# Kernel tuning notes

Measured on AMD Instinct MI355X. Metric: run time of the kernel, lower is better.

Reference implementation:

```python
import jax, jax.numpy as jnp
import numpy as np

H, C = 4, 32            # heads, hidden_channel
HC = H * C              # 128
IN = 128                # in_channel
N = 50000               # nodes in sampled subgraph
E = 200000              # edges
USER, ITEM = 50000, 50000
UB = 200                # ubias_num == ibias_num
DIST = 501
BATCH = 1024
NEG = 0.2               # leaky_relu negative slope


def setup_inputs() -> dict:
    key = jax.random.key(0)
    keys = iter(jax.random.split(key, 64))

    def nrm(shape):
        return jax.random.normal(next(keys), shape, dtype=jnp.float32) * 0.05

    def ri(shape, hi):
        return jax.random.randint(next(keys), shape, 0, hi, dtype=jnp.int32)

    inp = {
        # int (graph) inputs
        "node_idx": ri((N,), USER + ITEM + 1),
        "edge_index": ri((2, E), N),
        "edge_type": ri((E,), 6),
        "t_offset_0": ri((E,), UB + 2),
        "t_offset_1": ri((E,), UB + 2),
        "dists_0": ri((E,), DIST),
        "dists_1": ri((E,), DIST),
        "center_nid": ri((BATCH,), N),
        # parameters
        "id_emb": nrm((USER + ITEM + 1, IN)),
        "ucenter_att_bias": nrm((UB + 2, HC)),
        "icenter_att_bias": nrm((UB + 2, HC)),
        "trans_att_bias": nrm((UB + 2, HC)),
        "ucenter_emb_bias": nrm((UB + 2, HC)),
        "icenter_emb_bias": nrm((UB + 2, HC)),
        "trans_emb_bias": nrm((UB + 2, HC)),
        "ucenter_att_bias_2": nrm((UB * 4 + 2, HC)),
        "icenter_att_bias_2": nrm((UB * 4 + 2, HC)),
        "trans_att_bias_2": nrm((UB * 4 + 2, HC)),
        "ucenter_emb_bias_2": nrm((UB * 4 + 2, HC)),
        "icenter_emb_bias_2": nrm((UB * 4 + 2, HC)),
        "trans_emb_bias_2": nrm((UB * 4 + 2, HC)),
        "udist_att_bias": nrm((DIST, HC)),
        "idist_att_bias": nrm((DIST, HC)),
        "udist_emb_bias": nrm((DIST, HC)),
        "idist_emb_bias": nrm((DIST, HC)),
        "udist_att_bias_2": nrm((DIST, HC)),
        "idist_att_bias_2": nrm((DIST, HC)),
        "udist_emb_bias_2": nrm((DIST, HC)),
        "idist_emb_bias_2": nrm((DIST, HC)),
        "trans_head": nrm((IN, HC)),
        "rnn_w": nrm((2 * HC, HC)),           # rnn_update Linear (no bias)
        "w1": nrm((HC * 2 + IN, HC)),          # pred_head layer 1
        "b1": jnp.zeros((HC,), jnp.float32),
        "w2": nrm((HC, ITEM)),                 # pred_head layer 2
        "b2": jnp.zeros((ITEM,), jnp.float32),
        # per-layer conv params (src/dst projections + attention vectors)
        "wl0": nrm((IN, HC)), "wr0": nrm((IN, HC)),
        "asrc0": nrm((H, C)), "adst0": nrm((H, C)),
        "wl1": nrm((HC, HC)), "wr1": nrm((HC, HC)),
        "asrc1": nrm((H, C)), "adst1": nrm((H, C)),
    }
    return inp


def reference(node_idx, edge_index, edge_type, t_offset_0, t_offset_1, dists_0,
              dists_1, center_nid, id_emb, ucenter_att_bias, icenter_att_bias,
              trans_att_bias, ucenter_emb_bias, icenter_emb_bias, trans_emb_bias,
              ucenter_att_bias_2, icenter_att_bias_2, trans_att_bias_2,
              ucenter_emb_bias_2, icenter_emb_bias_2, trans_emb_bias_2,
              udist_att_bias, idist_att_bias, udist_emb_bias, idist_emb_bias,
              udist_att_bias_2, idist_att_bias_2, udist_emb_bias_2,
              idist_emb_bias_2, trans_head, rnn_w, w1, b1, w2, b2,
              wl0, wr0, asrc0, adst0, wl1, wr1, asrc1, adst1):
    x = id_emb[node_idx]                       # [N, IN] gather
    src, dst = edge_index[0], edge_index[1]
    is_u = (edge_type == 0)[:, None]           # user-center homo edges
    is_homo = (edge_type < 2)[:, None]
    involved = ((edge_type == 0) | (edge_type == 2) | (edge_type == 3))[:, None]

    def edge_bias(u_tab, i_tab, tr_tab, toff):
        # homo edges: type-0 -> user table, type-1 -> item table; hetero -> trans table
        b = jnp.where(is_u, u_tab[toff], jnp.where(is_homo, i_tab[toff], tr_tab[toff]))
        return b.reshape(-1, H, C)

    def dist_bias(u_tab, i_tab, dists):
        b = jnp.where(is_u, u_tab[dists], i_tab[dists]) * involved
        return b.reshape(-1, H, C)

    att_b = [edge_bias(ucenter_att_bias, icenter_att_bias, trans_att_bias, t_offset_0),
             edge_bias(ucenter_att_bias_2, icenter_att_bias_2, trans_att_bias_2, t_offset_1)]
    emb_b = [edge_bias(ucenter_emb_bias, icenter_emb_bias, trans_emb_bias, t_offset_0),
             edge_bias(ucenter_emb_bias_2, icenter_emb_bias_2, trans_emb_bias_2, t_offset_1)]
    att_d = [dist_bias(udist_att_bias, idist_att_bias, dists_0),
             dist_bias(udist_att_bias_2, idist_att_bias_2, dists_1)]
    emb_d = [dist_bias(udist_emb_bias, idist_emb_bias, dists_0),
             dist_bias(udist_emb_bias_2, idist_emb_bias_2, dists_1)]

    n_nodes = x.shape[0]

    def conv(h, wl, wr, asrc, adst, ab, eb, ad, ed):
        k = (h @ wl).reshape(n_nodes, H, C)
        q = (h @ wr).reshape(n_nodes, H, C)
        msg = k[src] + eb + ed                                   # [E,H,C]
        logit = jax.nn.leaky_relu(
            jnp.einsum('ehc,hc->eh', k[src] + ab + ad, asrc)
            + jnp.einsum('ehc,hc->eh', q[dst], adst), NEG)        # [E,H]
        m = jax.ops.segment_max(logit, dst, num_segments=n_nodes)
        a = jnp.exp(logit - m[dst])
        den = jax.ops.segment_sum(a, dst, num_segments=n_nodes)
        alpha = a / jnp.maximum(den[dst], 1e-16)
        out = jax.ops.segment_sum(alpha[..., None] * msg, dst, num_segments=n_nodes)
        return out.reshape(n_nodes, HC)

    layers = [(wl0, wr0, asrc0, adst0), (wl1, wr1, asrc1, adst1)]
    x_inter = [x]
    cur = x
    for i in range(2):
        last = cur @ trans_head if i == 0 else cur
        wl, wr, asrc, adst = layers[i]
        cur = conv(cur, wl, wr, asrc, adst, att_b[i], emb_b[i], att_d[i], emb_d[i])
        cur = jnp.tanh(jnp.concatenate([cur, last], axis=-1) @ rnn_w)
        x_inter.append(cur)
        if i != 1:
            cur = jax.nn.relu(cur)   # dropout: eval mode -> identity

    feat = jnp.concatenate(x_inter, axis=-1)[center_nid]   # [B, 2*HC+IN]
    hdd = jax.nn.leaky_relu(feat @ w1 + b1, NEG)            # dropout eval -> identity
    logits = hdd @ w2 + b2                                  # [B, ITEM]
    return logits
```

## Files before the change

kernel.cpp:

```cpp
#include <hip/hip_runtime.h>
#include <cstdint>
#include <cstddef>

typedef unsigned short u16;
typedef __attribute__((ext_vector_type(8))) short short8;
typedef __attribute__((ext_vector_type(4))) float f32x4;

#define HC_ 128
#define CAP 32
#define OFF_U0   0
#define OFF_I0   202
#define OFF_T0   404
#define OFF_UD0  606
#define OFF_ID0  1107
#define OFF_U2   1608
#define OFF_I2   2410
#define OFF_T2   3212
#define OFF_UD2  4014
#define OFF_ID2  4515
#define DOT_ROWS 5016

__device__ __forceinline__ float b2f(u16 u) {
  union { unsigned int i; float f; } v; v.i = ((unsigned int)u) << 16; return v.f;
}
__device__ __forceinline__ u16 f2b(float f) {
  union { float f; unsigned int i; } v; v.f = f;
  unsigned int r = v.i + 0x7fffu + ((v.i >> 16) & 1u);
  return (u16)(r >> 16);
}

__global__ __launch_bounds__(256) void prolog_k(
    const int* __restrict__ nidx, const float* __restrict__ emb, u16* __restrict__ x,
    const float* u0, const float* i0, const float* t0, const float* ud0, const float* id0,
    const float* u2, const float* i2, const float* t2, const float* ud2, const float* id2,
    const float* __restrict__ asrc0, const float* __restrict__ asrc1,
    float* __restrict__ dots,
    const float* __restrict__ wr0, const float* __restrict__ adst0,
    const float* __restrict__ wr1, const float* __restrict__ adst1,
    float* __restrict__ wq,
    const float* __restrict__ rnn_w, u16* __restrict__ rnn_wb,
    const float* __restrict__ th, u16* __restrict__ Wt,
    int* __restrict__ cur, float* __restrict__ kdot0, float* __restrict__ kdot1, int Nn)
{
  int b = blockIdx.x, t = threadIdx.x;
  const int nbCur  = (Nn + 255) >> 8;
  const int nbKd   = (Nn * 4 + 255) >> 8;
  const int nbGx   = (Nn * 16 + 255) >> 8;
  const int nbDots = (DOT_ROWS * 4 + 255) >> 8;

  if (b < nbCur) { int i = b * 256 + t; if (i < Nn) cur[i] = 0; return; }
  b -= nbCur;
  if (b < nbKd) {
    int i = b * 256 + t;
    if (i < Nn * 4) { kdot0[i] = 0.f; kdot1[i] = 0.f; }
    return;
  }
  b -= nbKd;
  if (b < nbGx) {
    int i = b * 256 + t;
    int n = i >> 4, c = (i & 15) << 3;
    if (n < Nn) {
      int id = nidx[n];
      const float* s = emb + (size_t)id * HC_ + c;
      u16 tmp[8];
#pragma unroll
      for (int j = 0; j < 8; ++j) tmp[j] = f2b(s[j]);
      *(short8*)(x + (size_t)n * HC_ + c) = *(short8*)tmp;
    }
    return;
  }
  b -= nbGx;
  if (b < nbDots) {
    int i = b * 256 + t;
    if (i < DOT_ROWS * 4) {
      int r = i >> 2, h = i & 3;
      const float* tab; int lr; const float* as;
      if      (r < OFF_I0)  { tab = u0;  lr = r;            as = asrc0; }
      else if (r < OFF_T0)  { tab = i0;  lr = r - OFF_I0;   as = asrc0; }
      else if (r < OFF_UD0) { tab = t0;  lr = r - OFF_T0;   as = asrc0; }
      else if (r < OFF_ID0) { tab = ud0; lr = r - OFF_UD0;  as = asrc0; }
      else if (r < OFF_U2)  { tab = id0; lr = r - OFF_ID0;  as = asrc0; }
      else if (r < OFF_I2)  { tab = u2;  lr = r - OFF_U2;   as = asrc1; }
      else if (r < OFF_T2)  { tab = i2;  lr = r - OFF_I2;   as = asrc1; }
      else if (r < OFF_UD2) { tab = t2;  lr = r - OFF_T2;   as = asrc1; }
      else if (r < OFF_ID2) { tab = ud2; lr = r - OFF_UD2;  as = asrc1; }
      else                  { tab = id2; lr = r - OFF_ID2;  as = asrc1; }
      float s = 0.f;
#pragma unroll
      for (int c = 0; c < 32; ++c)
        s += tab[(size_t)lr * HC_ + h * 32 + c] * as[h * 32 + c];
      dots[i] = s;
    }
    return;
  }
  b -= nbDots;
  if (b < 4) {
    int i = b * 256 + t;
    int layer = i >> 9, k = (i >> 2) & 127, h = i & 3;
    const float* wr = layer ? wr1 : wr0;
    const float* ad = layer ? adst1 : adst0;
    float s = 0.f;
#pragma unroll
    for (int c = 0; c < 32; ++c)
      s += wr[(size_t)k * HC_ + h * 32 + c] * ad[h * 32 + c];
    wq[i] = s;
    return;
  }
  b -= 4;
  if (b < 128) {
    int i = b * 256 + t;
    rnn_wb[i] = f2b(rnn_w[i]);
    return;
  }
  b -= 128;
  {
    int i = b * 256 + t;
    if (i < 16384) {
      int r = i >> 7, c = i & 127;
      float s = 0.f;
#pragma unroll 8
      for (int k = 0; k < 128; ++k)
        s += th[r * 128 + k] * rnn_w[(size_t)(128 + k) * 128 + c];
      Wt[i] = f2b(s);
    }
  }
}

__global__ void fill_k(const int* __restrict__ src, const int* __restrict__ dst,
                       const int* __restrict__ ety,
                       const int* __restrict__ toff0, const int* __restrict__ toff1,
                       const int* __restrict__ dist0, const int* __restrict__ dist1,
                       const float* __restrict__ dots,
                       int* __restrict__ cur,
                       int2* __restrict__ m0a, f32x4* __restrict__ e0a,
                       int2* __restrict__ m1a, f32x4* __restrict__ e1a, int E)
{
  int e = blockIdx.x * blockDim.x + threadIdx.x;
  if (e >= E) return;
  int d = dst[e];
  int slot = atomicAdd(&cur[d], 1);
  if (slot >= CAP) return;
  int s = src[e], ty = ety[e];
  int to0 = toff0[e], to1 = toff1[e], di0 = dist0[e], di1 = dist1[e];
  bool inv = (ty == 0 || ty == 2 || ty == 3);
  int ar0 = (ty == 0) ? (OFF_U0 + to0) : (ty < 2) ? (OFF_I0 + to0) : (OFF_T0 + to0);
  int ar1 = (ty == 0) ? (OFF_U2 + to1) : (ty < 2) ? (OFF_I2 + to1) : (OFF_T2 + to1);
  f32x4 e0 = *(const f32x4*)(dots + (size_t)ar0 * 4);
  f32x4 e1 = *(const f32x4*)(dots + (size_t)ar1 * 4);
  if (inv) {
    int dr0 = ((ty == 0) ? OFF_UD0 : OFF_ID0) + di0;
    int dr1 = ((ty == 0) ? OFF_UD2 : OFF_ID2) + di1;
    e0 += *(const f32x4*)(dots + (size_t)dr0 * 4);
    e1 += *(const f32x4*)(dots + (size_t)dr1 * 4);
  }
  size_t ix = (size_t)d * CAP + slot;
  m0a[ix] = make_int2(s, ty | (to0 << 3) | (di0 << 13));
  m1a[ix] = make_int2(s, ty | (to1 << 3) | (di1 << 13));
  e0a[ix] = e0;
  e1a[ix] = e1;
}

template<int EPI, int RELUA, int KS, int AF32, int OF32, int KQ>
__global__ __launch_bounds__(256) void gemm_k(
    const void* __restrict__ A_, const float* __restrict__ W,
    const float* __restrict__ bias, void* __restrict__ C_,
    const float* __restrict__ asrc, const float* __restrict__ wqt,
    float* __restrict__ kdot, float* __restrict__ qdot, int M, int N)
{
  const int lane = threadIdx.x & 63;
  const int wave = threadIdx.x >> 6;
  const int quad = lane >> 4;
  const int l16  = lane & 15;
  const int n0   = blockIdx.y * 64 + wave * 16;
  if (n0 >= N) return;

  short8 bfrag[KS];
#pragma unroll
  for (int ks = 0; ks < KS; ++ks) {
    short8 bf;
    const int kb = ks * 32 + quad * 8;
#pragma unroll
    for (int j = 0; j < 8; ++j)
      bf[j] = (short)f2b(W[(size_t)(kb + j) * N + n0 + l16]);
    bfrag[ks] = bf;
  }
  float bv = 0.f;
  if (EPI == 2 || EPI == 3) bv = bias[n0 + l16];

  const int mtiles = M >> 4;
  for (int mt = blockIdx.x; mt < mtiles; mt += gridDim.x) {
    f32x4 acc = {0.f, 0.f, 0.f, 0.f};
    float qp[4] = {0.f, 0.f, 0.f, 0.f};
    if (AF32) {
      const float* arow = (const float*)A_ + (size_t)(mt * 16 + l16) * (KS * 32);
#pragma unroll
      for (int ks = 0; ks < KS; ++ks) {
        short8 af;
#pragma unroll
        for (int j = 0; j < 8; ++j) {
          float v = arow[ks * 32 + quad * 8 + j];
          if (RELUA) v = fmaxf(v, 0.f);
          af[j] = (short)f2b(v);
        }
        acc = __builtin_amdgcn_mfma_f32_16x16x32_bf16(af, bfrag[ks], acc, 0, 0, 0);
      }
    } else {
      const u16* arow = (const u16*)A_ + (size_t)(mt * 16 + l16) * (KS * 32);
#pragma unroll
      for (int ks = 0; ks < KS; ++ks) {
        short8 af = *(const short8*)(arow + ks * 32 + quad * 8);
        if (RELUA) {
#pragma unroll
          for (int j = 0; j < 8; ++j) af[j] = (af[j] < (short)0) ? (short)0 : af[j];
        }
        if (KQ) {
#pragma unroll
          for (int j = 0; j < 8; ++j) {
            float v = b2f((u16)af[j]);
            const float* wr = wqt + (size_t)(ks * 32 + quad * 8 + j) * 4;
            qp[0] += v * wr[0]; qp[1] += v * wr[1];
            qp[2] += v * wr[2]; qp[3] += v * wr[3];
          }
        }
        acc = __builtin_amdgcn_mfma_f32_16x16x32_bf16(af, bfrag[ks], acc, 0, 0, 0);
      }
    }

    if (KQ) {
#pragma unroll
      for (int h = 0; h < 4; ++h) {
        qp[h] += __shfl_xor(qp[h], 16, 64);
        qp[h] += __shfl_xor(qp[h], 32, 64);
      }
      if (blockIdx.y == 0 && quad == 0) {
        f32x4 qv; qv[0] = qp[0]; qv[1] = qp[1]; qv[2] = qp[2]; qv[3] = qp[3];
        *(f32x4*)(qdot + (size_t)(mt * 16 + l16) * 4) = qv;
      }
      const int hh = n0 >> 5;
      const float asv = asrc[n0 + l16];
#pragma unroll
      for (int r = 0; r < 4; ++r) {
        float sr = acc[r] * asv;
        sr += __shfl_xor(sr, 1, 64); sr += __shfl_xor(sr, 2, 64);
        sr += __shfl_xor(sr, 4, 64); sr += __shfl_xor(sr, 8, 64);
        if (l16 == 0)
          atomicAdd(&kdot[(size_t)(mt * 16 + quad * 4 + r) * 4 + hh], sr);
      }
    }

#pragma unroll
    for (int r = 0; r < 4; ++r) {
      float v = acc[r];
      if (EPI == 2)      { v += bv; v = (v > 0.f) ? v : 0.2f * v; }
      else if (EPI == 3) { v += bv; }
      const size_t idx = (size_t)(mt * 16 + quad * 4 + r) * N + n0 + l16;
      if (OF32) ((float*)C_)[idx] = v;
      else      ((u16*)C_)[idx] = f2b(v);
    }
  }
}

__global__ __launch_bounds__(256) void gemm2_k(
    const float* __restrict__ A1, const u16* __restrict__ W1,
    const u16* __restrict__ A2, const u16* __restrict__ W2,
    u16* __restrict__ Cout, int M)
{
  const int lane = threadIdx.x & 63;
  const int wave = threadIdx.x >> 6;
  const int quad = lane >> 4;
  const int l16  = lane & 15;
  const int n0   = blockIdx.y * 64 + wave * 16;

  short8 bf1[4], bf2[4];
#pragma unroll
  for (int ks = 0; ks < 4; ++ks) {
    short8 a, b;
    const int kb = ks * 32 + quad * 8;
#pragma unroll
    for (int j = 0; j < 8; ++j) {
      a[j] = (short)W1[(size_t)(kb + j) * HC_ + n0 + l16];
      b[j] = (short)W2[(size_t)(kb + j) * HC_ + n0 + l16];
    }
    bf1[ks] = a; bf2[ks] = b;
  }

  const int mtiles = M >> 4;
  for (int mt = blockIdx.x; mt < mtiles; mt += gridDim.x) {
    const int rowm = mt * 16 + l16;
    const float* a1 = A1 + (size_t)rowm * HC_;
    const u16*   a2 = A2 + (size_t)rowm * HC_;
    f32x4 acc = {0.f, 0.f, 0.f, 0.f};
#pragma unroll
    for (int ks = 0; ks < 4; ++ks) {
      short8 af;
      const float* p = a1 + ks * 32 + quad * 8;
#pragma unroll
      for (int j = 0; j < 8; ++j) af[j] = (short)f2b(p[j]);
      acc = __builtin_amdgcn_mfma_f32_16x16x32_bf16(af, bf1[ks], acc, 0, 0, 0);
    }
#pragma unroll
    for (int ks = 0; ks < 4; ++ks) {
      short8 af = *(const short8*)(a2 + ks * 32 + quad * 8);
      acc = __builtin_amdgcn_mfma_f32_16x16x32_bf16(af, bf2[ks], acc, 0, 0, 0);
    }
#pragma unroll
    for (int r = 0; r < 4; ++r)
      Cout[(size_t)(mt * 16 + quad * 4 + r) * HC_ + n0 + l16] = f2b(tanhf(acc[r]));
  }
}

template<int MASKED>
__global__ __launch_bounds__(256) void conv_k(
    const int* __restrict__ cur, const int2* __restrict__ meta,
    const f32x4* __restrict__ edot,
    const u16* __restrict__ kbuf,
    const float* __restrict__ kdot, const float* __restrict__ qdot,
    const float* __restrict__ uemb, const float* __restrict__ iemb,
    const float* __restrict__ temb,
    const float* __restrict__ udemb, const float* __restrict__ idemb,
    const int* __restrict__ center, float* __restrict__ CO, int Ncnt)
{
  __shared__ float als[4][CAP][4];
  const int wv = threadIdx.x >> 6;
  int wid = (blockIdx.x * blockDim.x + threadIdx.x) >> 6;
  if (wid >= Ncnt) return;
  const int lane = threadIdx.x & 63;
  const int n = MASKED ? center[wid] : wid;
  int cnt = cur[n]; if (cnt > CAP) cnt = CAP;
  const int h0 = lane >> 5;
  const int h1 = h0 + 2;
  const float q0 = qdot[n * 4 + h0];
  const float q1 = qdot[n * 4 + h1];
  const int2* mb = meta + (size_t)n * CAP;
  const f32x4* eb = edot + (size_t)n * CAP;

  float den0 = 0.f, den1 = 0.f;
  for (int e = 0; e < cnt; ++e) {
    int s = mb[e].x;
    f32x4 ed = eb[e];
    float l0 = kdot[s * 4 + h0] + q0 + ed[h0];
    float l1 = kdot[s * 4 + h1] + q1 + ed[h1];
    l0 = (l0 > 0.f) ? l0 : 0.2f * l0;
    l1 = (l1 > 0.f) ? l1 : 0.2f * l1;
    float a0 = __expf(fminf(l0, 30.f));
    float a1 = __expf(fminf(l1, 30.f));
    den0 += a0; den1 += a1;
    if ((lane & 31) == 0) { als[wv][e][h0] = a0; als[wv][e][h1] = a1; }
  }
  const float r0 = 1.f / fmaxf(den0, 1e-16f);
  const float r1 = 1.f / fmaxf(den1, 1e-16f);

  float acc0 = 0.f, acc1 = 0.f;
  for (int e = 0; e < cnt; ++e) {
    int2 mrec = mb[e];
    int s = mrec.x;
    int ty = mrec.y & 7, to = (mrec.y >> 3) & 1023, di = mrec.y >> 13;
    float al0 = als[wv][e][h0] * r0;
    float al1 = als[wv][e][h1] * r1;

    float m0 = b2f(kbuf[(size_t)s * HC_ + lane]);
    float m1 = b2f(kbuf[(size_t)s * HC_ + 64 + lane]);
    const float* et = (ty == 0) ? uemb : (ty < 2) ? iemb : temb;
    m0 += et[(size_t)to * HC_ + lane];
    m1 += et[(size_t)to * HC_ + 64 + lane];
    if (ty == 0 || ty == 2 || ty == 3) {
      const float* dt = (ty == 0) ? udemb : idemb;
      m0 += dt[(size_t)di * HC_ + lane];
      m1 += dt[(size_t)di * HC_ + 64 + lane];
    }
    acc0 += al0 * m0;
    acc1 += al1 * m1;
  }
  CO[(size_t)n * HC_ + lane]      = acc0;
  CO[(size_t)n * HC_ + 64 + lane] = acc1;
}

__global__ __launch_bounds__(256) void gh_k(
    const float* __restrict__ CO, const u16* __restrict__ rnn_wb,
    const u16* __restrict__ h1, const u16* __restrict__ xb,
    const int* __restrict__ center, const float* __restrict__ w1,
    const float* __restrict__ b1, u16* __restrict__ hdd)
{
  __shared__ u16 h2s[16][136];
  const int t = threadIdx.x;
  const int lane = t & 63, wave = t >> 6, quad = lane >> 4, l16 = lane & 15;
  const int mt = blockIdx.x;
  const int rowm = mt * 16 + l16;
  const int nid = center[rowm];
  const u16* W1 = rnn_wb;
  const u16* W2 = rnn_wb + HC_ * HC_;

#pragma unroll
  for (int half = 0; half < 2; ++half) {
    const int n0 = half * 64 + wave * 16;
    short8 bf1[4], bf2[4];
#pragma unroll
    for (int ks = 0; ks < 4; ++ks) {
      short8 a, b;
      const int kb = ks * 32 + quad * 8;
#pragma unroll
      for (int j = 0; j < 8; ++j) {
        a[j] = (short)W1[(size_t)(kb + j) * HC_ + n0 + l16];
        b[j] = (short)W2[(size_t)(kb + j) * HC_ + n0 + l16];
      }
      bf1[ks] = a; bf2[ks] = b;
    }
    const float* a1 = CO + (size_t)nid * HC_;
    const u16*   a2 = h1 + (size_t)nid * HC_;
    f32x4 acc = {0.f, 0.f, 0.f, 0.f};
#pragma unroll
    for (int ks = 0; ks < 4; ++ks) {
      short8 af;
      const float* p = a1 + ks * 32 + quad * 8;
#pragma unroll
      for (int j = 0; j < 8; ++j) af[j] = (short)f2b(p[j]);
      acc = __builtin_amdgcn_mfma_f32_16x16x32_bf16(af, bf1[ks], acc, 0, 0, 0);
    }
#pragma unroll
    for (int ks = 0; ks < 4; ++ks) {
      short8 af = *(const short8*)(a2 + ks * 32 + quad * 8);
#pragma unroll
      for (int j = 0; j < 8; ++j) af[j] = (af[j] < (short)0) ? (short)0 : af[j];
      acc = __builtin_amdgcn_mfma_f32_16x16x32_bf16(af, bf2[ks], acc, 0, 0, 0);
    }
#pragma unroll
    for (int r = 0; r < 4; ++r)
      h2s[quad * 4 + r][n0 + l16] = f2b(tanhf(acc[r]));
  }
  __syncthreads();

#pragma unroll
  for (int half = 0; half < 2; ++half) {
    const int n0 = half * 64 + wave * 16;
    short8 bfrag[12];
#pragma unroll
    for (int ks = 0; ks < 12; ++ks) {
      short8 bf;
      const int kb = ks * 32 + quad * 8;
#pragma unroll
      for (int j = 0; j < 8; ++j)
        bf[j] = (short)f2b(w1[(size_t)(kb + j) * HC_ + n0 + l16]);
      bfrag[ks] = bf;
    }
    const float bv = b1[n0 + l16];
    f32x4 acc = {0.f, 0.f, 0.f, 0.f};
#pragma unroll
    for (int ks = 0; ks < 12; ++ks) {
      short8 af;
      if (ks < 4)
        af = *(const short8*)(xb + (size_t)nid * HC_ + ks * 32 + quad * 8);
      else if (ks < 8)
        af = *(const short8*)(h1 + (size_t)nid * HC_ + (ks - 4) * 32 + quad * 8);
      else
        af = *(const short8*)(&h2s[l16][(ks - 8) * 32 + quad * 8]);
      acc = __builtin_amdgcn_mfma_f32_16x16x32_bf16(af, bfrag[ks], acc, 0, 0, 0);
    }
#pragma unroll
    for (int r = 0; r < 4; ++r) {
      float v = acc[r] + bv;
      v = (v > 0.f) ? v : 0.2f * v;
      hdd[(size_t)(mt * 16 + quad * 4 + r) * HC_ + n0 + l16] = f2b(v);
    }
  }
}

__global__ __launch_bounds__(256) void gemm_out_k(
    const u16* __restrict__ A, const float* __restrict__ W,
    const float* __restrict__ bias, float* __restrict__ out, int M, int ITEM)
{
  __shared__ float lds[4][16][68];
  const int lane = threadIdx.x & 63;
  const int wv   = threadIdx.x >> 6;
  const int quad = lane >> 4;
  const int l16  = lane & 15;
  const int nbase = blockIdx.y * 256 + wv * 64;

  short8 bfrag[4][4];
#pragma unroll
  for (int nt = 0; nt < 4; ++nt) {
    const int colc = nbase + nt * 16 + l16;
    const int col = (colc < ITEM) ? colc : (ITEM - 1);
#pragma unroll
    for (int ks = 0; ks < 4; ++ks) {
      short8 bf;
      const int kb = ks * 32 + quad * 8;
#pragma unroll
      for (int j = 0; j < 8; ++j)
        bf[j] = (short)f2b(W[(size_t)(kb + j) * ITEM + col]);
      bfrag[nt][ks] = bf;
    }
  }
  const int c4 = nbase + l16 * 4;
  const bool wvalid = (c4 + 3) < ITEM;
  float4 bv = make_float4(0.f, 0.f, 0.f, 0.f);
  if (wvalid) bv = *(const float4*)(bias + c4);

  const int mtiles = M >> 4;
  for (int mt = blockIdx.x; mt < mtiles; mt += gridDim.x) {
    const u16* arow = A + (size_t)(mt * 16 + l16) * HC_;
    short8 af[4];
#pragma unroll
    for (int ks = 0; ks < 4; ++ks)
      af[ks] = *(const short8*)(arow + ks * 32 + quad * 8);
    f32x4 acc[4];
#pragma unroll
    for (int nt = 0; nt < 4; ++nt) acc[nt] = (f32x4){0.f, 0.f, 0.f, 0.f};
#pragma unroll
    for (int nt = 0; nt < 4; ++nt)
#pragma unroll
      for (int ks = 0; ks < 4; ++ks)
        acc[nt] = __builtin_amdgcn_mfma_f32_16x16x32_bf16(af[ks], bfrag[nt][ks],
                                                          acc[nt], 0, 0, 0);
#pragma unroll
    for (int nt = 0; nt < 4; ++nt)
#pragma unroll
      for (int r = 0; r < 4; ++r)
        lds[wv][quad * 4 + r][nt * 16 + l16] = acc[nt][r];
    __syncthreads();
    if (wvalid) {
#pragma unroll
      for (int i = 0; i < 4; ++i) {
        const int row = (lane >> 4) + i * 4;
        float4 v = *(const float4*)(&lds[wv][row][l16 * 4]);
        v.x += bv.x; v.y += bv.y; v.z += bv.z; v.w += bv.w;
        *(float4*)(out + (size_t)(mt * 16 + row) * ITEM + c4) = v;
      }
    }
    __syncthreads();
  }
}

extern "C" void kernel_launch(void* const* d_in, const int* in_sizes, int n_in,
                              void* d_out, int out_size, void* d_ws, size_t ws_size,
                              hipStream_t stream)
{
  (void)n_in; (void)out_size; (void)ws_size;
  const int* node_idx = (const int*)d_in[0];
  const int* eidx     = (const int*)d_in[1];
  const int* etype    = (const int*)d_in[2];
  const int* toff0    = (const int*)d_in[3];
  const int* toff1    = (const int*)d_in[4];
  const int* dist0    = (const int*)d_in[5];
  const int* dist1    = (const int*)d_in[6];
  const int* center   = (const int*)d_in[7];
  const float* id_emb   = (const float*)d_in[8];
  const float* u_att    = (const float*)d_in[9];
  const float* i_att    = (const float*)d_in[10];
  const float* t_att    = (const float*)d_in[11];
  const float* u_emb    = (const float*)d_in[12];
  const float* i_emb    = (const float*)d_in[13];
  const float* t_emb    = (const float*)d_in[14];
  const float* u_att2   = (const float*)d_in[15];
  const float* i_att2   = (const float*)d_in[16];
  const float* t_att2   = (const float*)d_in[17];
  const float* u_emb2   = (const float*)d_in[18];
  const float* i_emb2   = (const float*)d_in[19];
  const float* t_emb2   = (const float*)d_in[20];
  const float* ud_att   = (const float*)d_in[21];
  const float* id_att   = (const float*)d_in[22];
  const float* ud_emb   = (const float*)d_in[23];
  const float* id_embd  = (const float*)d_in[24];
  const float* ud_att2  = (const float*)d_in[25];
  const float* id_att2  = (const float*)d_in[26];
  const float* ud_emb2  = (const float*)d_in[27];
  const float* id_emb2  = (const float*)d_in[28];
  const float* trans_head = (const float*)d_in[29];
  const float* rnn_w    = (const float*)d_in[30];
  const float* w1       = (const float*)d_in[31];
  const float* b1       = (const float*)d_in[32];
  const float* w2       = (const float*)d_in[33];
  const float* b2       = (const float*)d_in[34];
  const float* wl0      = (const float*)d_in[35];
  const float* wr0      = (const float*)d_in[36];
  const float* asrc0    = (const float*)d_in[37];
  const float* adst0    = (const float*)d_in[38];
  const float* wl1      = (const float*)d_in[39];
  const float* wr1      = (const float*)d_in[40];
  const float* asrc1    = (const float*)d_in[41];
  const float* adst1    = (const float*)d_in[42];

  const int N_    = in_sizes[0];
  const int E_    = in_sizes[2];
  const int B_    = in_sizes[7];
  const int ITEM_ = in_sizes[34];
  const int* esrc = eidx;
  const int* edst = eidx + E_;

  char* ws = (char*)d_ws;
  size_t off = 0;
  auto alloc = [&](size_t bytes) -> char* {
    char* p = ws + off;
    off += (bytes + 255) & ~(size_t)255;
    return p;
  };
  float* CO_b  = (float*)alloc((size_t)N_ * HC_ * 4);
  u16*   k_b   = (u16*)  alloc((size_t)N_ * HC_ * 2);
  u16*   x_b   = (u16*)  alloc((size_t)N_ * HC_ * 2);
  u16*   h1_b  = (u16*)  alloc((size_t)N_ * HC_ * 2);
  float* kdot0 = (float*)alloc((size_t)N_ * 4 * 4);
  float* kdot1 = (float*)alloc((size_t)N_ * 4 * 4);
  float* qdot  = (float*)alloc((size_t)N_ * 4 * 4);
  float* dots  = (float*)alloc((size_t)DOT_ROWS * 4 * 4);
  float* wq    = (float*)alloc(1024 * 4);
  u16*   rnn_wb= (u16*)  alloc(256 * HC_ * 2);
  u16*   Wt    = (u16*)  alloc(HC_ * HC_ * 2);
  u16*   hdd   = (u16*)  alloc((size_t)B_ * HC_ * 2);
  int*   cur   = (int*)  alloc((size_t)N_ * 4);
  int2*  m0a   = (int2*) alloc((size_t)N_ * CAP * 8);
  int2*  m1a   = (int2*) alloc((size_t)N_ * CAP * 8);
  f32x4* e0a   = (f32x4*)alloc((size_t)N_ * CAP * 16);
  f32x4* e1a   = (f32x4*)alloc((size_t)N_ * CAP * 16);

  const int TB = 256;
  auto nb = [&](long long t) { return (int)((t + TB - 1) / TB); };

  const int nbCur  = (N_ + 255) / 256;
  const int nbKd   = (N_ * 4 + 255) / 256;
  const int nbGx   = (N_ * 16 + 255) / 256;
  const int nbDots = (DOT_ROWS * 4 + 255) / 256;
  const int prologBlocks = nbCur + nbKd + nbGx + nbDots + 4 + 128 + 64;
  prolog_k<<<prologBlocks, TB, 0, stream>>>(
      node_idx, id_emb, x_b,
      u_att, i_att, t_att, ud_att, id_att,
      u_att2, i_att2, t_att2, ud_att2, id_att2,
      asrc0, asrc1, dots,
      wr0, adst0, wr1, adst1, wq,
      rnn_w, rnn_wb, trans_head, Wt,
      cur, kdot0, kdot1, N_);

  fill_k<<<nb(E_), TB, 0, stream>>>(esrc, edst, etype, toff0, toff1, dist0, dist1,
                                    dots, cur, m0a, e0a, m1a, e1a, E_);

  gemm_k<0,0,4,0,0,1><<<dim3(640, 2), TB, 0, stream>>>(
      x_b, wl0, nullptr, k_b, asrc0, wq, kdot0, qdot, N_, HC_);

  conv_k<0><<<nb((long long)N_ * 64), TB, 0, stream>>>(
      cur, m0a, e0a, k_b, kdot0, qdot,
      u_emb, i_emb, t_emb, ud_emb, id_embd, nullptr, CO_b, N_);

  gemm2_k<<<dim3(640, 2), TB, 0, stream>>>(CO_b, rnn_wb, x_b, Wt, h1_b, N_);

  gemm_k<0,1,4,0,0,1><<<dim3(640, 2), TB, 0, stream>>>(
      h1_b, wl1, nullptr, k_b, asrc1, wq + 512, kdot1, qdot, N_, HC_);

  conv_k<1><<<nb((long long)B_ * 64), TB, 0, stream>>>(
      cur, m1a, e1a, k_b, kdot1, qdot,
      u_emb2, i_emb2, t_emb2, ud_emb2, id_emb2, center, CO_b, B_);

  gh_k<<<B_ / 16, TB, 0, stream>>>(CO_b, rnn_wb, h1_b, x_b, center, w1, b1, hdd);

  gemm_out_k<<<dim3(8, (ITEM_ + 255) / 256), TB, 0, stream>>>(
      hdd, w2, b2, (float*)d_out, B_, ITEM_);
}
```

Before: 634.8 us.

## Restrict GAT layers to receptive field of center nodes via frontier masks

Marks the nodes that actually influence the center-node outputs: centers, their 1-hop sources and their 2-hop sources. These are compacted into index lists, and the layer-0 GEMM, layer-0 conv, RNN GEMM and layer-1 GEMM run only over those rows instead of all N nodes. Padded rows at index N act as sentinels for partial tiles. This adds a memset, mark and compaction kernels plus gathered, indirect row access. Because CAP truncation applies only to the conv inputs, while marking uses every edge, some extra nodes are computed, which is still correct.

```diff
diff --git a/kernel.cpp b/kernel.cpp
--- a/kernel.cpp
+++ b/kernel.cpp
@@ -40,22 +40,33 @@
     float* __restrict__ wq,
     const float* __restrict__ rnn_w, u16* __restrict__ rnn_wb,
     const float* __restrict__ th, u16* __restrict__ Wt,
-    int* __restrict__ cur, float* __restrict__ kdot0, float* __restrict__ kdot1, int Nn)
+    int* __restrict__ cur, float* __restrict__ kdot0, float* __restrict__ kdot1,
+    int* __restrict__ mask1, int* __restrict__ mask2,
+    const int* __restrict__ center, int B_, int Nn)
 {
   int b = blockIdx.x, t = threadIdx.x;
-  const int nbCur  = (Nn + 255) >> 8;
-  const int nbKd   = (Nn * 4 + 255) >> 8;
-  const int nbGx   = (Nn * 16 + 255) >> 8;
+  const int nbZ    = (Nn + 16 + 255) >> 8;
+  const int nbC    = (B_ + 255) >> 8;
+  const int nbGx   = ((Nn + 16) * 16 + 255) >> 8;
   const int nbDots = (DOT_ROWS * 4 + 255) >> 8;
 
-  if (b < nbCur) { int i = b * 256 + t; if (i < Nn) cur[i] = 0; return; }
-  b -= nbCur;
-  if (b < nbKd) {
+  if (b < nbZ) {
     int i = b * 256 + t;
-    if (i < Nn * 4) { kdot0[i] = 0.f; kdot1[i] = 0.f; }
+    if (i < Nn + 16) {
+      cur[i] = 0;
+      f32x4 z = {0.f, 0.f, 0.f, 0.f};
+      *(f32x4*)(kdot0 + (size_t)i * 4) = z;
+      *(f32x4*)(kdot1 + (size_t)i * 4) = z;
+    }
     return;
   }
-  b -= nbKd;
+  b -= nbZ;
+  if (b < nbC) {
+    int i = b * 256 + t;
+    if (i < B_) { int c = center[i]; mask2[c] = 1; mask1[c] = 1; }
+    return;
+  }
+  b -= nbC;
   if (b < nbGx) {
     int i = b * 256 + t;
     int n = i >> 4, c = (i & 15) << 3;
@@ -66,6 +77,9 @@
 #pragma unroll
       for (int j = 0; j < 8; ++j) tmp[j] = f2b(s[j]);
       *(short8*)(x + (size_t)n * HC_ + c) = *(short8*)tmp;
+    } else if (n < Nn + 16) {
+      short8 z = {0,0,0,0,0,0,0,0};
+      *(short8*)(x + (size_t)n * HC_ + c) = z;
     }
     return;
   }
@@ -133,14 +147,17 @@
                        const float* __restrict__ dots,
                        int* __restrict__ cur,
                        int2* __restrict__ m0a, f32x4* __restrict__ e0a,
-                       int2* __restrict__ m1a, f32x4* __restrict__ e1a, int E)
+                       int2* __restrict__ m1a, f32x4* __restrict__ e1a,
+                       const int* __restrict__ mask2, int* __restrict__ mask1, int E)
 {
   int e = blockIdx.x * blockDim.x + threadIdx.x;
   if (e >= E) return;
   int d = dst[e];
+  int s = src[e];
+  if (mask2[d]) mask1[s] = 1;
   int slot = atomicAdd(&cur[d], 1);
   if (slot >= CAP) return;
-  int s = src[e], ty = ety[e];
+  int ty = ety[e];
   int to0 = toff0[e], to1 = toff1[e], di0 = dist0[e], di1 = dist1[e];
   bool inv = (ty == 0 || ty == 2 || ty == 3);
   int ar0 = (ty == 0) ? (OFF_U0 + to0) : (ty < 2) ? (OFF_I0 + to0) : (OFF_T0 + to0);
@@ -160,116 +177,115 @@
   e1a[ix] = e1;
 }
 
-template<int EPI, int RELUA, int KS, int AF32, int OF32, int KQ>
-__global__ __launch_bounds__(256) void gemm_k(
-    const void* __restrict__ A_, const float* __restrict__ W,
-    const float* __restrict__ bias, void* __restrict__ C_,
+__global__ void mark0_k(const int* __restrict__ esrc, const int* __restrict__ edst,
+                        const int* __restrict__ mask1, int* __restrict__ mask0, int E)
+{
+  int e = blockIdx.x * blockDim.x + threadIdx.x;
+  if (e < E && mask1[edst[e]]) mask0[esrc[e]] = 1;
+}
+
+__global__ void compact_k(const int* __restrict__ mask0, const int* __restrict__ mask1,
+                          int* __restrict__ L0, int* __restrict__ L1,
+                          int* __restrict__ cnts, int Nn)
+{
+  int n = blockIdx.x * blockDim.x + threadIdx.x;
+  if (n >= Nn) return;
+  int m1 = mask1[n];
+  if (m1 | mask0[n]) L0[atomicAdd(&cnts[0], 1)] = n;
+  if (m1)            L1[atomicAdd(&cnts[1], 1)] = n;
+}
+
+template<int RELUA>
+__global__ __launch_bounds__(256) void gemm_kq_g(
+    const u16* __restrict__ A, const float* __restrict__ W, u16* __restrict__ C,
     const float* __restrict__ asrc, const float* __restrict__ wqt,
-    float* __restrict__ kdot, float* __restrict__ qdot, int M, int N)
+    float* __restrict__ kdot, float* __restrict__ qdot,
+    const int* __restrict__ list, const int* __restrict__ cnts, int ci, int Nsent)
+{
+  const int lane = threadIdx.x & 63;
+  const int wave = threadIdx.x >> 6;
+  const int quad = lane >> 4;
+  const int l16  = lane & 15;
+  const int by   = blockIdx.y;
+  const int n0   = by * 64 + wave * 16;
+
+  short8 bfrag[4];
+#pragma unroll
+  for (int ks = 0; ks < 4; ++ks) {
+    short8 bf;
+    const int kb = ks * 32 + quad * 8;
+#pragma unroll
+    for (int j = 0; j < 8; ++j)
+      bf[j] = (short)f2b(W[(size_t)(kb + j) * HC_ + n0 + l16]);
+    bfrag[ks] = bf;
+  }
+  const int hh = n0 >> 5;
+  const float asv = asrc[n0 + l16];
+
+  const int cnt = cnts[ci];
+  const int mtiles = (cnt + 15) >> 4;
+  for (int mt = blockIdx.x; mt < mtiles; mt += gridDim.x) {
+    const int rA = mt * 16 + l16;
+    const int gA = (rA < cnt) ? list[rA] : Nsent;
+    const u16* arow = A + (size_t)gA * HC_;
+    f32x4 acc = {0.f, 0.f, 0.f, 0.f};
+    float qp[4] = {0.f, 0.f, 0.f, 0.f};
+#pragma unroll
+    for (int ks = 0; ks < 4; ++ks) {
+      short8 af = *(const short8*)(arow + ks * 32 + quad * 8);
+      if (RELUA) {
+#pragma unroll
+        for (int j = 0; j < 8; ++j) af[j] = (af[j] < (short)0) ? (short)0 : af[j];
+      }
+#pragma unroll
+      for (int j = 0; j < 8; ++j) {
+        float v = b2f((u16)af[j]);
+        const float* wr = wqt + (size_t)(ks * 32 + quad * 8 + j) * 4;
+        qp[0] += v * wr[0]; qp[1] += v * wr[1];
+        qp[2] += v * wr[2]; qp[3] += v * wr[3];
+      }
+      acc = __builtin_amdgcn_mfma_f32_16x16x32_bf16(af, bfrag[ks], acc, 0, 0, 0);
+    }
+#pragma unroll
+    for (int h = 0; h < 4; ++h) {
+      qp[h] += __shfl_xor(qp[h], 16, 64);
+      qp[h] += __shfl_xor(qp[h], 32, 64);
+    }
+    if (by == 0 && quad == 0) {
+      f32x4 qv; qv[0] = qp[0]; qv[1] = qp[1]; qv[2] = qp[2]; qv[3] = qp[3];
+      *(f32x4*)(qdot + (size_t)gA * 4) = qv;
+    }
+    int gC[4];
+#pragma unroll
+    for (int r = 0; r < 4; ++r) {
+      const int rC = mt * 16 + quad * 4 + r;
+      gC[r] = (rC < cnt) ? list[rC] : Nsent;
+    }
+#pragma unroll
+    for (int r = 0; r < 4; ++r) {
+      float sr = acc[r] * asv;
+      sr += __shfl_xor(sr, 1, 64); sr += __shfl_xor(sr, 2, 64);
+      sr += __shfl_xor(sr, 4, 64); sr += __shfl_xor(sr, 8, 64);
+      if (l16 == 0)
+        atomicAdd(&kdot[(size_t)gC[r] * 4 + hh], sr);
+    }
+#pragma unroll
+    for (int r = 0; r < 4; ++r)
+      C[(size_t)gC[r] * HC_ + n0 + l16] = f2b(acc[r]);
+  }
+}
+
+__global__ __launch_bounds__(256) void gemm2_g(
+    const float* __restrict__ A1, const u16* __restrict__ W1,
+    const u16* __restrict__ A2, const u16* __restrict__ W2,
+    u16* __restrict__ Cout,
+    const int* __restrict__ list, const int* __restrict__ cnts, int ci, int Nsent)
 {
   const int lane = threadIdx.x & 63;
   const int wave = threadIdx.x >> 6;
   const int quad = lane >> 4;
   const int l16  = lane & 15;
   const int n0   = blockIdx.y * 64 + wave * 16;
-  if (n0 >= N) return;
-
-  short8 bfrag[KS];
-#pragma unroll
-  for (int ks = 0; ks < KS; ++ks) {
-    short8 bf;
-    const int kb = ks * 32 + quad * 8;
-#pragma unroll
-    for (int j = 0; j < 8; ++j)
-      bf[j] = (short)f2b(W[(size_t)(kb + j) * N + n0 + l16]);
-    bfrag[ks] = bf;
-  }
-  float bv = 0.f;
-  if (EPI == 2 || EPI == 3) bv = bias[n0 + l16];
-
-  const int mtiles = M >> 4;
-  for (int mt = blockIdx.x; mt < mtiles; mt += gridDim.x) {
-    f32x4 acc = {0.f, 0.f, 0.f, 0.f};
-    float qp[4] = {0.f, 0.f, 0.f, 0.f};
-    if (AF32) {
-      const float* arow = (const float*)A_ + (size_t)(mt * 16 + l16) * (KS * 32);
-#pragma unroll
-      for (int ks = 0; ks < KS; ++ks) {
-        short8 af;
-#pragma unroll
-        for (int j = 0; j < 8; ++j) {
-          float v = arow[ks * 32 + quad * 8 + j];
-          if (RELUA) v = fmaxf(v, 0.f);
-          af[j] = (short)f2b(v);
-        }
-        acc = __builtin_amdgcn_mfma_f32_16x16x32_bf16(af, bfrag[ks], acc, 0, 0, 0);
-      }
-    } else {
-      const u16* arow = (const u16*)A_ + (size_t)(mt * 16 + l16) * (KS * 32);
-#pragma unroll
-      for (int ks = 0; ks < KS; ++ks) {
-        short8 af = *(const short8*)(arow + ks * 32 + quad * 8);
-        if (RELUA) {
-#pragma unroll
-          for (int j = 0; j < 8; ++j) af[j] = (af[j] < (short)0) ? (short)0 : af[j];
-        }
-        if (KQ) {
-#pragma unroll
-          for (int j = 0; j < 8; ++j) {
-            float v = b2f((u16)af[j]);
-            const float* wr = wqt + (size_t)(ks * 32 + quad * 8 + j) * 4;
-            qp[0] += v * wr[0]; qp[1] += v * wr[1];
-            qp[2] += v * wr[2]; qp[3] += v * wr[3];
-          }
-        }
-        acc = __builtin_amdgcn_mfma_f32_16x16x32_bf16(af, bfrag[ks], acc, 0, 0, 0);
-      }
-    }
-
-    if (KQ) {
-#pragma unroll
-      for (int h = 0; h < 4; ++h) {
-        qp[h] += __shfl_xor(qp[h], 16, 64);
-        qp[h] += __shfl_xor(qp[h], 32, 64);
-      }
-      if (blockIdx.y == 0 && quad == 0) {
-        f32x4 qv; qv[0] = qp[0]; qv[1] = qp[1]; qv[2] = qp[2]; qv[3] = qp[3];
-        *(f32x4*)(qdot + (size_t)(mt * 16 + l16) * 4) = qv;
-      }
-      const int hh = n0 >> 5;
-      const float asv = asrc[n0 + l16];
-#pragma unroll
-      for (int r = 0; r < 4; ++r) {
-        float sr = acc[r] * asv;
-        sr += __shfl_xor(sr, 1, 64); sr += __shfl_xor(sr, 2, 64);
-        sr += __shfl_xor(sr, 4, 64); sr += __shfl_xor(sr, 8, 64);
-        if (l16 == 0)
-          atomicAdd(&kdot[(size_t)(mt * 16 + quad * 4 + r) * 4 + hh], sr);
-      }
-    }
-
-#pragma unroll
-    for (int r = 0; r < 4; ++r) {
-      float v = acc[r];
-      if (EPI == 2)      { v += bv; v = (v > 0.f) ? v : 0.2f * v; }
-      else if (EPI == 3) { v += bv; }
-      const size_t idx = (size_t)(mt * 16 + quad * 4 + r) * N + n0 + l16;
-      if (OF32) ((float*)C_)[idx] = v;
-      else      ((u16*)C_)[idx] = f2b(v);
-    }
-  }
-}
-
-__global__ __launch_bounds__(256) void gemm2_k(
-    const float* __restrict__ A1, const u16* __restrict__ W1,
-    const u16* __restrict__ A2, const u16* __restrict__ W2,
-    u16* __restrict__ Cout, int M)
-{
-  const int lane = threadIdx.x & 63;
-  const int wave = threadIdx.x >> 6;
-  const int quad = lane >> 4;
-  const int l16  = lane & 15;
-  const int n0   = blockIdx.y * 64 + wave * 16;
 
   short8 bf1[4], bf2[4];
 #pragma unroll
@@ -284,11 +300,13 @@
     bf1[ks] = a; bf2[ks] = b;
   }
 
-  const int mtiles = M >> 4;
+  const int cnt = cnts[ci];
+  const int mtiles = (cnt + 15) >> 4;
   for (int mt = blockIdx.x; mt < mtiles; mt += gridDim.x) {
-    const int rowm = mt * 16 + l16;
-    const float* a1 = A1 + (size_t)rowm * HC_;
-    const u16*   a2 = A2 + (size_t)rowm * HC_;
+    const int rA = mt * 16 + l16;
+    const int gA = (rA < cnt) ? list[rA] : Nsent;
+    const float* a1 = A1 + (size_t)gA * HC_;
+    const u16*   a2 = A2 + (size_t)gA * HC_;
     f32x4 acc = {0.f, 0.f, 0.f, 0.f};
 #pragma unroll
     for (int ks = 0; ks < 4; ++ks) {
@@ -304,12 +322,15 @@
       acc = __builtin_amdgcn_mfma_f32_16x16x32_bf16(af, bf2[ks], acc, 0, 0, 0);
     }
 #pragma unroll
-    for (int r = 0; r < 4; ++r)
-      Cout[(size_t)(mt * 16 + quad * 4 + r) * HC_ + n0 + l16] = f2b(tanhf(acc[r]));
-  }
-}
-
-template<int MASKED>
+    for (int r = 0; r < 4; ++r) {
+      const int rC = mt * 16 + quad * 4 + r;
+      const int gC = (rC < cnt) ? list[rC] : Nsent;
+      Cout[(size_t)gC * HC_ + n0 + l16] = f2b(tanhf(acc[r]));
+    }
+  }
+}
+
+template<int DEVCNT>
 __global__ __launch_bounds__(256) void conv_k(
     const int* __restrict__ cur, const int2* __restrict__ meta,
     const f32x4* __restrict__ edot,
@@ -318,61 +339,65 @@
     const float* __restrict__ uemb, const float* __restrict__ iemb,
     const float* __restrict__ temb,
     const float* __restrict__ udemb, const float* __restrict__ idemb,
-    const int* __restrict__ center, float* __restrict__ CO, int Ncnt)
+    const int* __restrict__ list, const int* __restrict__ cnts, int ci, int cntConst,
+    float* __restrict__ CO)
 {
   __shared__ float als[4][CAP][4];
   const int wv = threadIdx.x >> 6;
-  int wid = (blockIdx.x * blockDim.x + threadIdx.x) >> 6;
-  if (wid >= Ncnt) return;
   const int lane = threadIdx.x & 63;
-  const int n = MASKED ? center[wid] : wid;
-  int cnt = cur[n]; if (cnt > CAP) cnt = CAP;
+  const int bound = DEVCNT ? cnts[ci] : cntConst;
+  const int wstep = gridDim.x * 4;
   const int h0 = lane >> 5;
   const int h1 = h0 + 2;
-  const float q0 = qdot[n * 4 + h0];
-  const float q1 = qdot[n * 4 + h1];
-  const int2* mb = meta + (size_t)n * CAP;
-  const f32x4* eb = edot + (size_t)n * CAP;
-
-  float den0 = 0.f, den1 = 0.f;
-  for (int e = 0; e < cnt; ++e) {
-    int s = mb[e].x;
-    f32x4 ed = eb[e];
-    float l0 = kdot[s * 4 + h0] + q0 + ed[h0];
-    float l1 = kdot[s * 4 + h1] + q1 + ed[h1];
-    l0 = (l0 > 0.f) ? l0 : 0.2f * l0;
-    l1 = (l1 > 0.f) ? l1 : 0.2f * l1;
-    float a0 = __expf(fminf(l0, 30.f));
-    float a1 = __expf(fminf(l1, 30.f));
-    den0 += a0; den1 += a1;
-    if ((lane & 31) == 0) { als[wv][e][h0] = a0; als[wv][e][h1] = a1; }
-  }
-  const float r0 = 1.f / fmaxf(den0, 1e-16f);
-  const float r1 = 1.f / fmaxf(den1, 1e-16f);
-
-  float acc0 = 0.f, acc1 = 0.f;
-  for (int e = 0; e < cnt; ++e) {
-    int2 mrec = mb[e];
-    int s = mrec.x;
-    int ty = mrec.y & 7, to = (mrec.y >> 3) & 1023, di = mrec.y >> 13;
-    float al0 = als[wv][e][h0] * r0;
-    float al1 = als[wv][e][h1] * r1;
-
-    float m0 = b2f(kbuf[(size_t)s * HC_ + lane]);
-    float m1 = b2f(kbuf[(size_t)s * HC_ + 64 + lane]);
-    const float* et = (ty == 0) ? uemb : (ty < 2) ? iemb : temb;
-    m0 += et[(size_t)to * HC_ + lane];
-    m1 += et[(size_t)to * HC_ + 64 + lane];
-    if (ty == 0 || ty == 2 || ty == 3) {
-      const float* dt = (ty == 0) ? udemb : idemb;
-      m0 += dt[(size_t)di * HC_ + lane];
-      m1 += dt[(size_t)di * HC_ + 64 + lane];
-    }
-    acc0 += al0 * m0;
-    acc1 += al1 * m1;
-  }
-  CO[(size_t)n * HC_ + lane]      = acc0;
-  CO[(size_t)n * HC_ + 64 + lane] = acc1;
+
+  for (int wid = (blockIdx.x * blockDim.x + threadIdx.x) >> 6; wid < bound; wid += wstep) {
+    const int n = list[wid];
+    int cnt = cur[n]; if (cnt > CAP) cnt = CAP;
+    const float q0 = qdot[n * 4 + h0];
+    const float q1 = qdot[n * 4 + h1];
+    const int2* mb = meta + (size_t)n * CAP;
+    const f32x4* eb = edot + (size_t)n * CAP;
+
+    float den0 = 0.f, den1 = 0.f;
+    for (int e = 0; e < cnt; ++e) {
+      int s = mb[e].x;
+      f32x4 ed = eb[e];
+      float l0 = kdot[s * 4 + h0] + q0 + ed[h0];
+      float l1 = kdot[s * 4 + h1] + q1 + ed[h1];
+      l0 = (l0 > 0.f) ? l0 : 0.2f * l0;
+      l1 = (l1 > 0.f) ? l1 : 0.2f * l1;
+      float a0 = __expf(fminf(l0, 30.f));
+      float a1 = __expf(fminf(l1, 30.f));
+      den0 += a0; den1 += a1;
+      if ((lane & 31) == 0) { als[wv][e][h0] = a0; als[wv][e][h1] = a1; }
+    }
+    const float r0 = 1.f / fmaxf(den0, 1e-16f);
+    const float r1 = 1.f / fmaxf(den1, 1e-16f);
+
+    float acc0 = 0.f, acc1 = 0.f;
+    for (int e = 0; e < cnt; ++e) {
+      int2 mrec = mb[e];
+      int s = mrec.x;
+      int ty = mrec.y & 7, to = (mrec.y >> 3) & 1023, di = mrec.y >> 13;
+      float al0 = als[wv][e][h0] * r0;
+      float al1 = als[wv][e][h1] * r1;
+
+      float m0 = b2f(kbuf[(size_t)s * HC_ + lane]);
+      float m1 = b2f(kbuf[(size_t)s * HC_ + 64 + lane]);
+      const float* et = (ty == 0) ? uemb : (ty < 2) ? iemb : temb;
+      m0 += et[(size_t)to * HC_ + lane];
+      m1 += et[(size_t)to * HC_ + 64 + lane];
+      if (ty == 0 || ty == 2 || ty == 3) {
+        const float* dt = (ty == 0) ? udemb : idemb;
+        m0 += dt[(size_t)di * HC_ + lane];
+        m1 += dt[(size_t)di * HC_ + 64 + lane];
+      }
+      acc0 += al0 * m0;
+      acc1 += al1 * m1;
+    }
+    CO[(size_t)n * HC_ + lane]      = acc0;
+    CO[(size_t)n * HC_ + 64 + lane] = acc1;
+  }
 }
 
 __global__ __launch_bounds__(256) void gh_k(
@@ -593,32 +618,42 @@
     off += (bytes + 255) & ~(size_t)255;
     return p;
   };
-  float* CO_b  = (float*)alloc((size_t)N_ * HC_ * 4);
-  u16*   k_b   = (u16*)  alloc((size_t)N_ * HC_ * 2);
-  u16*   x_b   = (u16*)  alloc((size_t)N_ * HC_ * 2);
-  u16*   h1_b  = (u16*)  alloc((size_t)N_ * HC_ * 2);
-  float* kdot0 = (float*)alloc((size_t)N_ * 4 * 4);
-  float* kdot1 = (float*)alloc((size_t)N_ * 4 * 4);
-  float* qdot  = (float*)alloc((size_t)N_ * 4 * 4);
+  const int NS = N_ + 16;
+  float* CO_b  = (float*)alloc((size_t)NS * HC_ * 4);
+  u16*   k_b   = (u16*)  alloc((size_t)NS * HC_ * 2);
+  u16*   x_b   = (u16*)  alloc((size_t)NS * HC_ * 2);
+  u16*   h1_b  = (u16*)  alloc((size_t)NS * HC_ * 2);
+  float* kdot0 = (float*)alloc((size_t)NS * 4 * 4);
+  float* kdot1 = (float*)alloc((size_t)NS * 4 * 4);
+  float* qdot  = (float*)alloc((size_t)NS * 4 * 4);
   float* dots  = (float*)alloc((size_t)DOT_ROWS * 4 * 4);
   float* wq    = (float*)alloc(1024 * 4);
   u16*   rnn_wb= (u16*)  alloc(256 * HC_ * 2);
   u16*   Wt    = (u16*)  alloc(HC_ * HC_ * 2);
   u16*   hdd   = (u16*)  alloc((size_t)B_ * HC_ * 2);
-  int*   cur   = (int*)  alloc((size_t)N_ * 4);
+  int*   cur   = (int*)  alloc((size_t)NS * 4);
   int2*  m0a   = (int2*) alloc((size_t)N_ * CAP * 8);
   int2*  m1a   = (int2*) alloc((size_t)N_ * CAP * 8);
   f32x4* e0a   = (f32x4*)alloc((size_t)N_ * CAP * 16);
   f32x4* e1a   = (f32x4*)alloc((size_t)N_ * CAP * 16);
+  int*   maskb = (int*)  alloc(((size_t)3 * N_ + 2) * 4);
+  int*   mask0 = maskb;
+  int*   mask1 = maskb + N_;
+  int*   mask2 = maskb + 2 * N_;
+  int*   cnts  = maskb + 3 * N_;
+  int*   L0    = (int*)  alloc((size_t)N_ * 4);
+  int*   L1    = (int*)  alloc((size_t)N_ * 4);
 
   const int TB = 256;
   auto nb = [&](long long t) { return (int)((t + TB - 1) / TB); };
 
-  const int nbCur  = (N_ + 255) / 256;
-  const int nbKd   = (N_ * 4 + 255) / 256;
-  const int nbGx   = (N_ * 16 + 255) / 256;
+  hipMemsetAsync(maskb, 0, ((size_t)3 * N_ + 2) * 4, stream);
+
+  const int nbZ    = (N_ + 16 + 255) / 256;
+  const int nbC    = (B_ + 255) / 256;
+  const int nbGx   = ((N_ + 16) * 16 + 255) / 256;
   const int nbDots = (DOT_ROWS * 4 + 255) / 256;
-  const int prologBlocks = nbCur + nbKd + nbGx + nbDots + 4 + 128 + 64;
+  const int prologBlocks = nbZ + nbC + nbGx + nbDots + 4 + 128 + 64;
   prolog_k<<<prologBlocks, TB, 0, stream>>>(
       node_idx, id_emb, x_b,
       u_att, i_att, t_att, ud_att, id_att,
@@ -626,26 +661,31 @@
       asrc0, asrc1, dots,
       wr0, adst0, wr1, adst1, wq,
       rnn_w, rnn_wb, trans_head, Wt,
-      cur, kdot0, kdot1, N_);
+      cur, kdot0, kdot1,
+      mask1, mask2, center, B_, N_);
 
   fill_k<<<nb(E_), TB, 0, stream>>>(esrc, edst, etype, toff0, toff1, dist0, dist1,
-                                    dots, cur, m0a, e0a, m1a, e1a, E_);
-
-  gemm_k<0,0,4,0,0,1><<<dim3(640, 2), TB, 0, stream>>>(
-      x_b, wl0, nullptr, k_b, asrc0, wq, kdot0, qdot, N_, HC_);
-
-  conv_k<0><<<nb((long long)N_ * 64), TB, 0, stream>>>(
+                                    dots, cur, m0a, e0a, m1a, e1a, mask2, mask1, E_);
+
+  mark0_k<<<nb(E_), TB, 0, stream>>>(esrc, edst, mask1, mask0, E_);
+  compact_k<<<nb(N_), TB, 0, stream>>>(mask0, mask1, L0, L1, cnts, N_);
+
+  gemm_kq_g<0><<<dim3(640, 2), TB, 0, stream>>>(
+      x_b, wl0, k_b, asrc0, wq, kdot0, qdot, L0, cnts, 0, N_);
+
+  conv_k<1><<<1536, TB, 0, stream>>>(
       cur, m0a, e0a, k_b, kdot0, qdot,
-      u_emb, i_emb, t_emb, ud_emb, id_embd, nullptr, CO_b, N_);
-
-  gemm2_k<<<dim3(640, 2), TB, 0, stream>>>(CO_b, rnn_wb, x_b, Wt, h1_b, N_);
-
-  gemm_k<0,1,4,0,0,1><<<dim3(640, 2), TB, 0, stream>>>(
-      h1_b, wl1, nullptr, k_b, asrc1, wq + 512, kdot1, qdot, N_, HC_);
-
-  conv_k<1><<<nb((long long)B_ * 64), TB, 0, stream>>>(
+      u_emb, i_emb, t_emb, ud_emb, id_embd, L1, cnts, 1, 0, CO_b);
+
+  gemm2_g<<<dim3(640, 2), TB, 0, stream>>>(CO_b, rnn_wb, x_b, Wt, h1_b,
+                                           L1, cnts, 1, N_);
+
+  gemm_kq_g<1><<<dim3(640, 2), TB, 0, stream>>>(
+      h1_b, wl1, k_b, asrc1, wq + 512, kdot1, qdot, L1, cnts, 1, N_);
+
+  conv_k<0><<<nb((long long)B_ * 64), TB, 0, stream>>>(
       cur, m1a, e1a, k_b, kdot1, qdot,
-      u_emb2, i_emb2, t_emb2, ud_emb2, id_emb2, center, CO_b, B_);
+      u_emb2, i_emb2, t_emb2, ud_emb2, id_emb2, center, nullptr, 0, B_, CO_b);
 
   gh_k<<<B_ / 16, TB, 0, stream>>>(CO_b, rnn_wb, h1_b, x_b, center, w1, b1, hdd);
 
```

Result: faster. 559.5 us (-11.9%).
